# Optimization experiments

Hardware: AMD Instinct MI355X
Metric: run time of the kernel (lower is better)

## Reference

```python
import jax, jax.numpy as jnp
import numpy as np

H = 128
M = 50000
L = 400000
EPS = 1e-9


def setup_inputs() -> dict:
    key = jax.random.key(0)
    ks = jax.random.split(key, 24)
    d = {
        'x_emb': jax.random.normal(ks[0], (M, H), jnp.float32),
        'child_h': jax.random.normal(ks[1], (M, H), jnp.float32),
        'child_c': jax.random.normal(ks[2], (M, H), jnp.float32),
        'pair_cand_idx': jax.random.randint(ks[3], (L,), 0, M, jnp.int32),
        'pair_child_idx': jax.random.randint(ks[4], (L,), 0, M, jnp.int32),
    }
    s = 1.0 / np.sqrt(H)
    names = ['Wi_w', 'Ui_w', 'Wf_w', 'Uf_w', 'Wo_w', 'Uo_w', 'Wc_w', 'Uc_w', 'Wa_w', 'Ua_w']
    for i, n in enumerate(names):
        d[n] = jax.random.uniform(ks[5 + i], (H, H), jnp.float32, -s, s)
    for i, n in enumerate(['Wi_b', 'Wf_b', 'Wo_b', 'Wc_b', 'Wa_b']):
        d[n] = jax.random.uniform(ks[15 + i], (H,), jnp.float32, -s, s)
    d['v_w'] = jax.random.uniform(ks[20], (H,), jnp.float32, -s, s)
    return d


def reference(x_emb, child_h, child_c, pair_cand_idx, pair_child_idx,
              Wi_w, Ui_w, Wf_w, Uf_w, Wo_w, Uo_w, Wc_w, Uc_w, Wa_w, Ua_w,
              Wi_b, Wf_b, Wo_b, Wc_b, Wa_b, v_w):
    m = x_emb.shape[0]
    ci, chi = pair_cand_idx, pair_child_idx

    # --- segment attention (torch version runs under no_grad) ---
    Ah = child_h @ Wa_w.T + Wa_b          # [M,H]
    Bx = x_emb @ Ua_w.T                   # [M,H]
    e = jnp.tanh(Ah[chi] + Bx[ci]) @ v_w  # [L]
    seg_max = jax.ops.segment_max(e, ci, num_segments=m)
    x_exp = jnp.exp(e - seg_max[ci])
    seg_sum = jax.ops.segment_sum(x_exp, ci, num_segments=m) + EPS
    attn = x_exp / seg_sum[ci]            # [L]
    h_hat = jax.ops.segment_sum(attn[:, None] * child_h[chi], ci, num_segments=m)  # [M,H]

    # --- tree-LSTM gates ---
    i_j = jax.nn.sigmoid(x_emb @ Wi_w.T + Wi_b + h_hat @ Ui_w.T)
    Wfx = x_emb @ Wf_w.T + Wf_b
    Ufh = child_h @ Uf_w.T
    f_pair = jax.nn.sigmoid(Wfx[ci] + Ufh[chi])                       # [L,H]
    sum_f_c = jax.ops.segment_sum(f_pair * child_c[chi], ci, num_segments=m)
    c_t = jnp.tanh(x_emb @ Wc_w.T + Wc_b + h_hat @ Uc_w.T)
    c = i_j * c_t + sum_f_c
    o_j = jax.nn.sigmoid(x_emb @ Wo_w.T + Wo_b + h_hat @ Uo_w.T)
    h = o_j * jnp.tanh(c)
    return (h, c)
```

## Files before the change

kernel.cpp:

```cpp
#include <hip/hip_runtime.h>
#include <cstdint>
#include <cstddef>

#define H 128

typedef __bf16 v8bf __attribute__((ext_vector_type(8)));
typedef __bf16 v4bf __attribute__((ext_vector_type(4)));
typedef float  v4f  __attribute__((ext_vector_type(4)));

__device__ __forceinline__ float ftanh(float x) {
    return 1.f - 2.f / (1.f + __expf(2.f * x));
}
__device__ __forceinline__ float fsigm(float x) {
    return 1.f / (1.f + __expf(-x));
}

struct MatDesc {
    const __bf16* A;
    const float*  W;
    const float*  bias;
    __bf16*       C;
};
struct MatBatch { MatDesc m[7]; };

__global__ __launch_bounds__(256) void convert_k(const float* __restrict__ x,
                                                 const float* __restrict__ chh,
                                                 __bf16* __restrict__ xe,
                                                 __bf16* __restrict__ che,
                                                 int MH4, int* __restrict__ counts, int M) {
    int i = blockIdx.x * 256 + threadIdx.x;
    if (i < MH4) {
        v4f a = ((const v4f*)x)[i];
        v4f b = ((const v4f*)chh)[i];
        v4bf ab, bb;
#pragma unroll
        for (int k = 0; k < 4; ++k) { ab[k] = (__bf16)a[k]; bb[k] = (__bf16)b[k]; }
        ((v4bf*)xe)[i] = ab;
        ((v4bf*)che)[i] = bb;
    }
    if (i < M) counts[i] = 0;
}

__global__ __launch_bounds__(256) void gemm_batch(MatBatch batch, int M) {
    const MatDesc d = batch.m[blockIdx.y];
    __shared__ __bf16 wlds[H][H + 8];

    for (int i = threadIdx.x; i < H * H; i += 256)
        wlds[i >> 7][i & 127] = (__bf16)d.W[i];
    __syncthreads();

    const int wave = threadIdx.x >> 6;
    const int lane = threadIdx.x & 63;
    const int quad = lane >> 4;
    const int l16  = lane & 15;
    const int r0   = blockIdx.x * 64 + wave * 16;

    v4f acc[8];
#pragma unroll
    for (int nt = 0; nt < 8; ++nt) acc[nt] = (v4f){0.f, 0.f, 0.f, 0.f};

    const __bf16* arow = d.A + (size_t)(r0 + l16) * H + quad * 8;
#pragma unroll
    for (int k0 = 0; k0 < H; k0 += 32) {
        v8bf a = *(const v8bf*)(arow + k0);
#pragma unroll
        for (int nt = 0; nt < 8; ++nt) {
            v8bf b = *(const v8bf*)(&wlds[nt * 16 + l16][k0 + quad * 8]);
            acc[nt] = __builtin_amdgcn_mfma_f32_16x16x32_bf16(a, b, acc[nt], 0, 0, 0);
        }
    }

#pragma unroll
    for (int nt = 0; nt < 8; ++nt) {
        int n = nt * 16 + l16;
        float bia = d.bias ? d.bias[n] : 0.f;
#pragma unroll
        for (int r = 0; r < 4; ++r) {
            int m = r0 + quad * 4 + r;
            if (m < M) d.C[(size_t)m * H + n] = (__bf16)(acc[nt][r] + bia);
        }
    }
}

__global__ __launch_bounds__(256) void edge_e(const __bf16* __restrict__ Ah,
                                              const __bf16* __restrict__ Bx,
                                              const int* __restrict__ ci,
                                              const int* __restrict__ chi,
                                              const float* __restrict__ vw,
                                              float* __restrict__ expe,
                                              int* __restrict__ counts, int L) {
    int tid = threadIdx.x;
    int sub = tid & 15;
    int l = blockIdx.x * 16 + (tid >> 4);
    if (l >= L) return;
    int c = ci[l], ch = chi[l];
    v8bf a = *(const v8bf*)(Ah + (size_t)ch * H + sub * 8);
    v8bf b = *(const v8bf*)(Bx + (size_t)c * H + sub * 8);
    v4f v0 = *(const v4f*)(vw + sub * 8);
    v4f v1 = *(const v4f*)(vw + sub * 8 + 4);
    float s = 0.f;
#pragma unroll
    for (int k = 0; k < 8; ++k) {
        float x = (float)a[k] + (float)b[k];
        float vv = (k < 4) ? v0[k] : v1[k - 4];
        s += ftanh(x) * vv;
    }
    s += __shfl_xor(s, 1);
    s += __shfl_xor(s, 2);
    s += __shfl_xor(s, 4);
    s += __shfl_xor(s, 8);
    if (sub == 0) {
        expe[l] = __expf(s);
        atomicAdd(&counts[c], 1);
    }
}

__global__ __launch_bounds__(1024) void scan_local(const int* __restrict__ counts,
                                                   int* __restrict__ excl,
                                                   int* __restrict__ bsums, int M) {
    __shared__ int s[1024];
    int tid = threadIdx.x;
    int idx = blockIdx.x * 1024 + tid;
    int v = (idx < M) ? counts[idx] : 0;
    s[tid] = v;
    __syncthreads();
    for (int off = 1; off < 1024; off <<= 1) {
        int t = (tid >= off) ? s[tid - off] : 0;
        __syncthreads();
        s[tid] += t;
        __syncthreads();
    }
    if (idx < M) excl[idx] = s[tid] - v;
    if (tid == 1023) bsums[blockIdx.x] = s[1023];
}

__global__ __launch_bounds__(1024) void scan_tops(const int* __restrict__ bsums,
                                                  int* __restrict__ boffs, int nb) {
    __shared__ int s[1024];
    int tid = threadIdx.x;
    int v = (tid < nb) ? bsums[tid] : 0;
    s[tid] = v;
    __syncthreads();
    for (int off = 1; off < 1024; off <<= 1) {
        int t = (tid >= off) ? s[tid - off] : 0;
        __syncthreads();
        s[tid] += t;
        __syncthreads();
    }
    if (tid < nb) boffs[tid] = s[tid] - v;
}

__global__ __launch_bounds__(1024) void scan_add(int* __restrict__ rowptr,
                                                 int* __restrict__ cursor,
                                                 const int* __restrict__ boffs,
                                                 const int* __restrict__ counts, int M) {
    int idx = blockIdx.x * 1024 + threadIdx.x;
    if (idx < M) {
        int v = rowptr[idx] + boffs[blockIdx.x];
        rowptr[idx] = v;
        cursor[idx] = v;
        if (idx == M - 1) rowptr[M] = v + counts[M - 1];
    }
}

__global__ __launch_bounds__(256) void scatter_k(const int* __restrict__ ci,
                                                 int* __restrict__ cursor,
                                                 int* __restrict__ edge_list, int L) {
    int l = blockIdx.x * 256 + threadIdx.x;
    if (l < L) {
        int pos = atomicAdd(&cursor[ci[l]], 1);
        edge_list[pos] = l;
    }
}

__global__ __launch_bounds__(128) void segment_k(const int* __restrict__ rowptr,
                                                 const int* __restrict__ edge_list,
                                                 const int* __restrict__ chi,
                                                 const float* __restrict__ expe,
                                                 const __bf16* __restrict__ Wfx,
                                                 const __bf16* __restrict__ Ufh,
                                                 const __bf16* __restrict__ ch16,
                                                 const float* __restrict__ child_c,
                                                 __bf16* __restrict__ hhat,
                                                 float* __restrict__ sumfc, int M) {
    int m = blockIdx.x;
    int h = threadIdx.x;
    int start = rowptr[m], deg = rowptr[m + 1] - start;
    __shared__ float red[128];
    __shared__ int   sch[128];
    __shared__ float sa[128];

    float part = 0.f;
    for (int j = h; j < deg; j += 128) part += expe[edge_list[start + j]];
    red[h] = part;
    __syncthreads();
#pragma unroll
    for (int s = 64; s > 0; s >>= 1) {
        if (h < s) red[h] += red[h + s];
        __syncthreads();
    }
    float inv = 1.f / (red[0] + 1e-9f);
    __syncthreads();

    float wfx = (float)Wfx[(size_t)m * H + h];
    float acch = 0.f, accf = 0.f;

    for (int base = 0; base < deg; base += 128) {
        int n = deg - base; if (n > 128) n = 128;
        if (h < n) {
            int l = edge_list[start + base + h];
            sch[h] = chi[l];
            sa[h]  = expe[l] * inv;
        }
        __syncthreads();
        int j = 0;
        for (; j + 1 < n; j += 2) {
            int c0 = sch[j], c1 = sch[j + 1];
            size_t r0 = (size_t)c0 * H + h, r1 = (size_t)c1 * H + h;
            float h0 = (float)ch16[r0], h1 = (float)ch16[r1];
            float u0 = (float)Ufh[r0],  u1 = (float)Ufh[r1];
            float cc0 = child_c[r0],    cc1 = child_c[r1];
            acch += sa[j] * h0 + sa[j + 1] * h1;
            accf += fsigm(wfx + u0) * cc0 + fsigm(wfx + u1) * cc1;
        }
        if (j < n) {
            int c0 = sch[j];
            size_t r0 = (size_t)c0 * H + h;
            acch += sa[j] * (float)ch16[r0];
            accf += fsigm(wfx + (float)Ufh[r0]) * child_c[r0];
        }
        __syncthreads();
    }
    hhat[(size_t)m * H + h] = (__bf16)acch;
    sumfc[(size_t)m * H + h] = accf;
}

__global__ __launch_bounds__(256) void final_k(const __bf16* __restrict__ Xi, const __bf16* __restrict__ Hi,
                                               const __bf16* __restrict__ Xc, const __bf16* __restrict__ Hc,
                                               const __bf16* __restrict__ Xo, const __bf16* __restrict__ Ho,
                                               const float* __restrict__ sumfc,
                                               float* __restrict__ out, int MH4, int MH) {
    int i = blockIdx.x * 256 + threadIdx.x;
    if (i >= MH4) return;
    v4bf xi = ((const v4bf*)Xi)[i], hi = ((const v4bf*)Hi)[i];
    v4bf xc = ((const v4bf*)Xc)[i], hc = ((const v4bf*)Hc)[i];
    v4bf xo = ((const v4bf*)Xo)[i], ho = ((const v4bf*)Ho)[i];
    v4f sf = ((const v4f*)sumfc)[i];
    v4f hout, cout;
#pragma unroll
    for (int k = 0; k < 4; ++k) {
        float ig = fsigm((float)xi[k] + (float)hi[k]);
        float ct = ftanh((float)xc[k] + (float)hc[k]);
        float og = fsigm((float)xo[k] + (float)ho[k]);
        float c = ig * ct + sf[k];
        cout[k] = c;
        hout[k] = og * ftanh(c);
    }
    ((v4f*)out)[i] = hout;
    ((v4f*)(out + MH))[i] = cout;
}

extern "C" void kernel_launch(void* const* d_in, const int* in_sizes, int n_in,
                              void* d_out, int out_size, void* d_ws, size_t ws_size,
                              hipStream_t stream) {
    const float* x_emb   = (const float*)d_in[0];
    const float* child_h = (const float*)d_in[1];
    const float* child_c = (const float*)d_in[2];
    const int*   ci      = (const int*)d_in[3];
    const int*   chi     = (const int*)d_in[4];
    const float* Wi_w = (const float*)d_in[5];
    const float* Ui_w = (const float*)d_in[6];
    const float* Wf_w = (const float*)d_in[7];
    const float* Uf_w = (const float*)d_in[8];
    const float* Wo_w = (const float*)d_in[9];
    const float* Uo_w = (const float*)d_in[10];
    const float* Wc_w = (const float*)d_in[11];
    const float* Uc_w = (const float*)d_in[12];
    const float* Wa_w = (const float*)d_in[13];
    const float* Ua_w = (const float*)d_in[14];
    const float* Wi_b = (const float*)d_in[15];
    const float* Wf_b = (const float*)d_in[16];
    const float* Wo_b = (const float*)d_in[17];
    const float* Wc_b = (const float*)d_in[18];
    const float* Wa_b = (const float*)d_in[19];
    const float* vw   = (const float*)d_in[20];

    const int M    = in_sizes[0] / H;
    const int L    = in_sizes[3];
    const int Mpad = (M + 63) & ~63;
    const int MH   = M * H;

    char* p = (char*)d_ws;
    auto alloc = [&](size_t bytes) {
        char* r = p;
        p += (bytes + 255) & ~(size_t)255;
        return (void*)r;
    };
    size_t bfbytes = (size_t)Mpad * H * sizeof(__bf16);
    __bf16* xe16   = (__bf16*)alloc(bfbytes);
    __bf16* ch16   = (__bf16*)alloc(bfbytes);
    __bf16* hhat16 = (__bf16*)alloc(bfbytes);
    __bf16* Ah16   = (__bf16*)alloc(bfbytes);
    __bf16* Bx16   = (__bf16*)alloc(bfbytes);
    __bf16* Wfx16  = (__bf16*)alloc(bfbytes);
    __bf16* Ufh16  = (__bf16*)alloc(bfbytes);
    __bf16* Xi16   = (__bf16*)alloc(bfbytes);
    __bf16* Xc16   = (__bf16*)alloc(bfbytes);
    __bf16* Xo16   = (__bf16*)alloc(bfbytes);
    float* sumfc     = (float*)alloc((size_t)MH * 4);
    float* expe      = (float*)alloc((size_t)L * 4);
    int*   edge_list = (int*)alloc((size_t)L * 4);
    int*   counts    = (int*)alloc((size_t)M * 4);
    int*   rowptr    = (int*)alloc((size_t)(M + 1) * 4);
    int*   cursor    = (int*)alloc((size_t)M * 4);
    int*   bsums     = (int*)alloc(1024 * 4);
    int*   boffs     = (int*)alloc(1024 * 4);
    __bf16* Hi16 = Ah16;
    __bf16* Hc16 = Bx16;
    __bf16* Ho16 = Wfx16;

    const int MH4 = MH / 4;
    convert_k<<<(MH4 + 255) / 256, 256, 0, stream>>>(x_emb, child_h, xe16, ch16, MH4, counts, M);

    MatBatch ba{};
    ba.m[0] = MatDesc{ch16, Wa_w, Wa_b, Ah16};
    ba.m[1] = MatDesc{xe16, Ua_w, nullptr, Bx16};
    ba.m[2] = MatDesc{xe16, Wf_w, Wf_b, Wfx16};
    ba.m[3] = MatDesc{ch16, Uf_w, nullptr, Ufh16};
    ba.m[4] = MatDesc{xe16, Wi_w, Wi_b, Xi16};
    ba.m[5] = MatDesc{xe16, Wc_w, Wc_b, Xc16};
    ba.m[6] = MatDesc{xe16, Wo_w, Wo_b, Xo16};
    dim3 gA(Mpad / 64, 7);
    gemm_batch<<<gA, 256, 0, stream>>>(ba, M);

    edge_e<<<(L + 15) / 16, 256, 0, stream>>>(Ah16, Bx16, ci, chi, vw, expe, counts, L);

    int nb = (M + 1023) / 1024;
    scan_local<<<nb, 1024, 0, stream>>>(counts, rowptr, bsums, M);
    scan_tops<<<1, 1024, 0, stream>>>(bsums, boffs, nb);
    scan_add<<<nb, 1024, 0, stream>>>(rowptr, cursor, boffs, counts, M);

    scatter_k<<<(L + 255) / 256, 256, 0, stream>>>(ci, cursor, edge_list, L);
    segment_k<<<M, 128, 0, stream>>>(rowptr, edge_list, chi, expe, Wfx16, Ufh16, ch16, child_c,
                                     hhat16, sumfc, M);

    MatBatch bb{};
    bb.m[0] = MatDesc{hhat16, Ui_w, nullptr, Hi16};
    bb.m[1] = MatDesc{hhat16, Uc_w, nullptr, Hc16};
    bb.m[2] = MatDesc{hhat16, Uo_w, nullptr, Ho16};
    dim3 gB(Mpad / 64, 3);
    gemm_batch<<<gB, 256, 0, stream>>>(bb, M);

    final_k<<<(MH4 + 255) / 256, 256, 0, stream>>>(Xi16, Hi16, Xc16, Hc16, Xo16, Ho16, sumfc,
                                                   (float*)d_out, MH4, MH);
}
```

Baseline: 435.1 us.

## Interleave child h/c/Ufh rows and use wave-per-segment gather

Packs bf16 child_h, bf16 child_c and the Ufh GEMM output into one interleaved row of stride 384, so each gathered child touches one contiguous region instead of three separate arrays. segment_k now assigns 32 lanes per segment, each handling 4 features with vector loads and shuffle reductions, which replaces the block-wide shared-memory reductions and barriers. Weights are pre-converted to bf16 once so GEMM blocks load them with vector copies. child_c is now rounded to bf16, which loses some accuracy.

```diff
diff --git a/kernel.cpp b/kernel.cpp
--- a/kernel.cpp
+++ b/kernel.cpp
@@ -3,6 +3,7 @@
 #include <cstddef>
 
 #define H 128
+#define PSTRIDE 384
 
 typedef __bf16 v8bf __attribute__((ext_vector_type(8)));
 typedef __bf16 v4bf __attribute__((ext_vector_type(4)));
@@ -17,26 +18,49 @@
 
 struct MatDesc {
     const __bf16* A;
-    const float*  W;
+    int           lda;
+    const __bf16* Wb;
     const float*  bias;
     __bf16*       C;
+    int           ldc;
 };
 struct MatBatch { MatDesc m[7]; };
+struct WPtrs { const float* w[10]; };
+
+__global__ __launch_bounds__(256) void wconv(WPtrs wp, __bf16* __restrict__ Wb) {
+    int i = blockIdx.x * 256 + threadIdx.x;
+    if (i >= 10 * 4096) return;
+    int mat = i >> 12;
+    int off = (i & 4095) << 2;
+    v4f a = *(const v4f*)(wp.w[mat] + off);
+    v4bf b;
+#pragma unroll
+    for (int k = 0; k < 4; ++k) b[k] = (__bf16)a[k];
+    *(v4bf*)(Wb + mat * 16384 + off) = b;
+}
 
 __global__ __launch_bounds__(256) void convert_k(const float* __restrict__ x,
                                                  const float* __restrict__ chh,
+                                                 const float* __restrict__ chc,
                                                  __bf16* __restrict__ xe,
-                                                 __bf16* __restrict__ che,
+                                                 __bf16* __restrict__ P,
                                                  int MH4, int* __restrict__ counts, int M) {
     int i = blockIdx.x * 256 + threadIdx.x;
     if (i < MH4) {
         v4f a = ((const v4f*)x)[i];
         v4f b = ((const v4f*)chh)[i];
-        v4bf ab, bb;
-#pragma unroll
-        for (int k = 0; k < 4; ++k) { ab[k] = (__bf16)a[k]; bb[k] = (__bf16)b[k]; }
+        v4f c = ((const v4f*)chc)[i];
+        v4bf ab, bb, cb;
+#pragma unroll
+        for (int k = 0; k < 4; ++k) {
+            ab[k] = (__bf16)a[k]; bb[k] = (__bf16)b[k]; cb[k] = (__bf16)c[k];
+        }
         ((v4bf*)xe)[i] = ab;
-        ((v4bf*)che)[i] = bb;
+        int m = i >> 5;
+        int q = (i & 31) << 2;
+        __bf16* prow = P + (size_t)m * PSTRIDE + q;
+        *(v4bf*)prow = bb;
+        *(v4bf*)(prow + H) = cb;
     }
     if (i < M) counts[i] = 0;
 }
@@ -45,8 +69,11 @@
     const MatDesc d = batch.m[blockIdx.y];
     __shared__ __bf16 wlds[H][H + 8];
 
-    for (int i = threadIdx.x; i < H * H; i += 256)
-        wlds[i >> 7][i & 127] = (__bf16)d.W[i];
+    for (int t = threadIdx.x; t < 2048; t += 256) {
+        int n = t >> 4;
+        int k = (t & 15) << 3;
+        *(v8bf*)&wlds[n][k] = *(const v8bf*)(d.Wb + n * H + k);
+    }
     __syncthreads();
 
     const int wave = threadIdx.x >> 6;
@@ -59,7 +86,7 @@
 #pragma unroll
     for (int nt = 0; nt < 8; ++nt) acc[nt] = (v4f){0.f, 0.f, 0.f, 0.f};
 
-    const __bf16* arow = d.A + (size_t)(r0 + l16) * H + quad * 8;
+    const __bf16* arow = d.A + (size_t)(r0 + l16) * d.lda + quad * 8;
 #pragma unroll
     for (int k0 = 0; k0 < H; k0 += 32) {
         v8bf a = *(const v8bf*)(arow + k0);
@@ -77,7 +104,7 @@
 #pragma unroll
         for (int r = 0; r < 4; ++r) {
             int m = r0 + quad * 4 + r;
-            if (m < M) d.C[(size_t)m * H + n] = (__bf16)(acc[nt][r] + bia);
+            if (m < M) d.C[(size_t)m * d.ldc + n] = (__bf16)(acc[nt][r] + bia);
         }
     }
 }
@@ -178,61 +205,74 @@
                                                  const int* __restrict__ chi,
                                                  const float* __restrict__ expe,
                                                  const __bf16* __restrict__ Wfx,
-                                                 const __bf16* __restrict__ Ufh,
-                                                 const __bf16* __restrict__ ch16,
-                                                 const float* __restrict__ child_c,
+                                                 const __bf16* __restrict__ P,
                                                  __bf16* __restrict__ hhat,
                                                  float* __restrict__ sumfc, int M) {
-    int m = blockIdx.x;
-    int h = threadIdx.x;
+    int g    = threadIdx.x >> 5;
+    int lane = threadIdx.x & 31;
+    int m = blockIdx.x * 4 + g;
+    if (m >= M) return;
     int start = rowptr[m], deg = rowptr[m + 1] - start;
-    __shared__ float red[128];
-    __shared__ int   sch[128];
-    __shared__ float sa[128];
 
     float part = 0.f;
-    for (int j = h; j < deg; j += 128) part += expe[edge_list[start + j]];
-    red[h] = part;
-    __syncthreads();
-#pragma unroll
-    for (int s = 64; s > 0; s >>= 1) {
-        if (h < s) red[h] += red[h + s];
-        __syncthreads();
-    }
-    float inv = 1.f / (red[0] + 1e-9f);
-    __syncthreads();
-
-    float wfx = (float)Wfx[(size_t)m * H + h];
-    float acch = 0.f, accf = 0.f;
-
-    for (int base = 0; base < deg; base += 128) {
-        int n = deg - base; if (n > 128) n = 128;
-        if (h < n) {
-            int l = edge_list[start + base + h];
-            sch[h] = chi[l];
-            sa[h]  = expe[l] * inv;
+    for (int j = lane; j < deg; j += 32) part += expe[edge_list[start + j]];
+    part += __shfl_xor(part, 1);
+    part += __shfl_xor(part, 2);
+    part += __shfl_xor(part, 4);
+    part += __shfl_xor(part, 8);
+    part += __shfl_xor(part, 16);
+    float inv = 1.f / (part + 1e-9f);
+
+    int h = lane << 2;
+    v4bf wf4 = *(const v4bf*)(Wfx + (size_t)m * H + h);
+    float wfx[4];
+#pragma unroll
+    for (int k = 0; k < 4; ++k) wfx[k] = (float)wf4[k];
+
+    float acch[4] = {0.f, 0.f, 0.f, 0.f};
+    float accf[4] = {0.f, 0.f, 0.f, 0.f};
+
+    int j = 0;
+    for (; j + 1 < deg; j += 2) {
+        int l0 = edge_list[start + j], l1 = edge_list[start + j + 1];
+        int c0 = chi[l0], c1 = chi[l1];
+        float a0 = expe[l0] * inv, a1 = expe[l1] * inv;
+        const __bf16* p0 = P + c0 * PSTRIDE + h;
+        const __bf16* p1 = P + c1 * PSTRIDE + h;
+        v4bf h0 = *(const v4bf*)p0;
+        v4bf c4_0 = *(const v4bf*)(p0 + H);
+        v4bf u0 = *(const v4bf*)(p0 + 2 * H);
+        v4bf h1 = *(const v4bf*)p1;
+        v4bf c4_1 = *(const v4bf*)(p1 + H);
+        v4bf u1 = *(const v4bf*)(p1 + 2 * H);
+#pragma unroll
+        for (int k = 0; k < 4; ++k) {
+            acch[k] += a0 * (float)h0[k] + a1 * (float)h1[k];
+            accf[k] += fsigm(wfx[k] + (float)u0[k]) * (float)c4_0[k]
+                     + fsigm(wfx[k] + (float)u1[k]) * (float)c4_1[k];
         }
-        __syncthreads();
-        int j = 0;
-        for (; j + 1 < n; j += 2) {
-            int c0 = sch[j], c1 = sch[j + 1];
-            size_t r0 = (size_t)c0 * H + h, r1 = (size_t)c1 * H + h;
-            float h0 = (float)ch16[r0], h1 = (float)ch16[r1];
-            float u0 = (float)Ufh[r0],  u1 = (float)Ufh[r1];
-            float cc0 = child_c[r0],    cc1 = child_c[r1];
-            acch += sa[j] * h0 + sa[j + 1] * h1;
-            accf += fsigm(wfx + u0) * cc0 + fsigm(wfx + u1) * cc1;
+    }
+    if (j < deg) {
+        int l0 = edge_list[start + j];
+        int c0 = chi[l0];
+        float a0 = expe[l0] * inv;
+        const __bf16* p0 = P + c0 * PSTRIDE + h;
+        v4bf h0 = *(const v4bf*)p0;
+        v4bf c4_0 = *(const v4bf*)(p0 + H);
+        v4bf u0 = *(const v4bf*)(p0 + 2 * H);
+#pragma unroll
+        for (int k = 0; k < 4; ++k) {
+            acch[k] += a0 * (float)h0[k];
+            accf[k] += fsigm(wfx[k] + (float)u0[k]) * (float)c4_0[k];
         }
-        if (j < n) {
-            int c0 = sch[j];
-            size_t r0 = (size_t)c0 * H + h;
-            acch += sa[j] * (float)ch16[r0];
-            accf += fsigm(wfx + (float)Ufh[r0]) * child_c[r0];
-        }
-        __syncthreads();
-    }
-    hhat[(size_t)m * H + h] = (__bf16)acch;
-    sumfc[(size_t)m * H + h] = accf;
+    }
+
+    v4bf hb;
+    v4f sf;
+#pragma unroll
+    for (int k = 0; k < 4; ++k) { hb[k] = (__bf16)acch[k]; sf[k] = accf[k]; }
+    *(v4bf*)(hhat + (size_t)m * H + h) = hb;
+    *(v4f*)(sumfc + (size_t)m * H + h) = sf;
 }
 
 __global__ __launch_bounds__(256) void final_k(const __bf16* __restrict__ Xi, const __bf16* __restrict__ Hi,
@@ -268,16 +308,6 @@
     const float* child_c = (const float*)d_in[2];
     const int*   ci      = (const int*)d_in[3];
     const int*   chi     = (const int*)d_in[4];
-    const float* Wi_w = (const float*)d_in[5];
-    const float* Ui_w = (const float*)d_in[6];
-    const float* Wf_w = (const float*)d_in[7];
-    const float* Uf_w = (const float*)d_in[8];
-    const float* Wo_w = (const float*)d_in[9];
-    const float* Uo_w = (const float*)d_in[10];
-    const float* Wc_w = (const float*)d_in[11];
-    const float* Uc_w = (const float*)d_in[12];
-    const float* Wa_w = (const float*)d_in[13];
-    const float* Ua_w = (const float*)d_in[14];
     const float* Wi_b = (const float*)d_in[15];
     const float* Wf_b = (const float*)d_in[16];
     const float* Wo_b = (const float*)d_in[17];
@@ -298,15 +328,15 @@
     };
     size_t bfbytes = (size_t)Mpad * H * sizeof(__bf16);
     __bf16* xe16   = (__bf16*)alloc(bfbytes);
-    __bf16* ch16   = (__bf16*)alloc(bfbytes);
+    __bf16* P      = (__bf16*)alloc((size_t)Mpad * PSTRIDE * sizeof(__bf16));
     __bf16* hhat16 = (__bf16*)alloc(bfbytes);
     __bf16* Ah16   = (__bf16*)alloc(bfbytes);
     __bf16* Bx16   = (__bf16*)alloc(bfbytes);
     __bf16* Wfx16  = (__bf16*)alloc(bfbytes);
-    __bf16* Ufh16  = (__bf16*)alloc(bfbytes);
     __bf16* Xi16   = (__bf16*)alloc(bfbytes);
     __bf16* Xc16   = (__bf16*)alloc(bfbytes);
     __bf16* Xo16   = (__bf16*)alloc(bfbytes);
+    __bf16* Wb     = (__bf16*)alloc(10 * 16384 * sizeof(__bf16));
     float* sumfc     = (float*)alloc((size_t)MH * 4);
     float* expe      = (float*)alloc((size_t)L * 4);
     int*   edge_list = (int*)alloc((size_t)L * 4);
@@ -319,17 +349,32 @@
     __bf16* Hc16 = Bx16;
     __bf16* Ho16 = Wfx16;
 
+    WPtrs wp;
+    for (int k = 0; k < 10; ++k) wp.w[k] = (const float*)d_in[5 + k];
+    wconv<<<(10 * 4096 + 255) / 256, 256, 0, stream>>>(wp, Wb);
+
     const int MH4 = MH / 4;
-    convert_k<<<(MH4 + 255) / 256, 256, 0, stream>>>(x_emb, child_h, xe16, ch16, MH4, counts, M);
+    convert_k<<<(MH4 + 255) / 256, 256, 0, stream>>>(x_emb, child_h, child_c, xe16, P, MH4, counts, M);
+
+    const __bf16* Wi = Wb + 0 * 16384;
+    const __bf16* Ui = Wb + 1 * 16384;
+    const __bf16* Wf = Wb + 2 * 16384;
+    const __bf16* Uf = Wb + 3 * 16384;
+    const __bf16* Wo = Wb + 4 * 16384;
+    const __bf16* Uo = Wb + 5 * 16384;
+    const __bf16* Wc = Wb + 6 * 16384;
+    const __bf16* Uc = Wb + 7 * 16384;
+    const __bf16* Wa = Wb + 8 * 16384;
+    const __bf16* Ua = Wb + 9 * 16384;
 
     MatBatch ba{};
-    ba.m[0] = MatDesc{ch16, Wa_w, Wa_b, Ah16};
-    ba.m[1] = MatDesc{xe16, Ua_w, nullptr, Bx16};
-    ba.m[2] = MatDesc{xe16, Wf_w, Wf_b, Wfx16};
-    ba.m[3] = MatDesc{ch16, Uf_w, nullptr, Ufh16};
-    ba.m[4] = MatDesc{xe16, Wi_w, Wi_b, Xi16};
-    ba.m[5] = MatDesc{xe16, Wc_w, Wc_b, Xc16};
-    ba.m[6] = MatDesc{xe16, Wo_w, Wo_b, Xo16};
+    ba.m[0] = MatDesc{P,    PSTRIDE, Wa, Wa_b,    Ah16,    H};
+    ba.m[1] = MatDesc{xe16, H,       Ua, nullptr, Bx16,    H};
+    ba.m[2] = MatDesc{xe16, H,       Wf, Wf_b,    Wfx16,   H};
+    ba.m[3] = MatDesc{P,    PSTRIDE, Uf, nullptr, P + 2*H, PSTRIDE};
+    ba.m[4] = MatDesc{xe16, H,       Wi, Wi_b,    Xi16,    H};
+    ba.m[5] = MatDesc{xe16, H,       Wc, Wc_b,    Xc16,    H};
+    ba.m[6] = MatDesc{xe16, H,       Wo, Wo_b,    Xo16,    H};
     dim3 gA(Mpad / 64, 7);
     gemm_batch<<<gA, 256, 0, stream>>>(ba, M);
 
@@ -341,13 +386,13 @@
     scan_add<<<nb, 1024, 0, stream>>>(rowptr, cursor, boffs, counts, M);
 
     scatter_k<<<(L + 255) / 256, 256, 0, stream>>>(ci, cursor, edge_list, L);
-    segment_k<<<M, 128, 0, stream>>>(rowptr, edge_list, chi, expe, Wfx16, Ufh16, ch16, child_c,
-                                     hhat16, sumfc, M);
+    segment_k<<<(M + 3) / 4, 128, 0, stream>>>(rowptr, edge_list, chi, expe, Wfx16, P,
+                                               hhat16, sumfc, M);
 
     MatBatch bb{};
-    bb.m[0] = MatDesc{hhat16, Ui_w, nullptr, Hi16};
-    bb.m[1] = MatDesc{hhat16, Uc_w, nullptr, Hc16};
-    bb.m[2] = MatDesc{hhat16, Uo_w, nullptr, Ho16};
+    bb.m[0] = MatDesc{hhat16, H, Ui, nullptr, Hi16, H};
+    bb.m[1] = MatDesc{hhat16, H, Uc, nullptr, Hc16, H};
+    bb.m[2] = MatDesc{hhat16, H, Uo, nullptr, Ho16, H};
     dim3 gB(Mpad / 64, 3);
     gemm_batch<<<gB, 256, 0, stream>>>(bb, M);
 
```

New measurement: 402.3 us. 1.08x faster.
